# Optimization experiments

Measured on AMD Instinct MI355X. Metric: run time of the kernel, lower is better.

## Reference

```python
import jax, jax.numpy as jnp
import numpy as np

B, T, D_IN, D_OUT = 4, 2048, 1024, 1024


def setup_inputs() -> dict:
    key = jax.random.key(0)
    k0, k1, k2, k3 = jax.random.split(key, 4)
    token_embed = jax.random.normal(k0, (B, T, D_IN), dtype=jnp.float32)
    # torch Linear weight is [out, in]; store transposed [in, out] for x @ W
    Wq = jax.random.normal(k1, (D_IN, D_OUT), dtype=jnp.float32) * (1.0 / np.sqrt(D_IN))
    Wk = jax.random.normal(k2, (D_IN, D_OUT), dtype=jnp.float32) * (1.0 / np.sqrt(D_IN))
    Wv = jax.random.normal(k3, (D_IN, D_OUT), dtype=jnp.float32) * (1.0 / np.sqrt(D_IN))
    return {"token_embed": token_embed, "Wq": Wq, "Wk": Wk, "Wv": Wv}


def reference(token_embed, Wq, Wk, Wv):
    # token_embed: [B, T, d_in]
    num_token = token_embed.shape[1]
    q = jnp.einsum("btd,de->bte", token_embed, Wq)  # [B, T, d_out]
    k = jnp.einsum("btd,de->bte", token_embed, Wk)
    v = jnp.einsum("btd,de->bte", token_embed, Wv)
    scores = jnp.einsum("bqe,bke->bqk", q, k)  # [B, T, T]
    # causal mask: strictly-upper-triangular positions set to -inf
    causal = jnp.triu(jnp.ones((num_token, num_token), dtype=bool), k=1)
    scores = jnp.where(causal[None, :, :], -jnp.inf, scores)
    # NOTE: faithful to source bug: scale by sqrt(seq_len) (keys.shape[1]), not sqrt(d_out)
    scale = jnp.asarray(num_token, dtype=scores.dtype) ** 0.5
    attn = jax.nn.softmax(scores / scale, axis=-1)
    # dropout prob is 0 -> identity
    context = jnp.einsum("bqk,bke->bqe", attn, v)  # [B, T, d_out]
    return context
```

## Files before the change

kernel.cpp:

```cpp
#include <hip/hip_runtime.h>
#include <cstdint>
#include <cstddef>
#include <math.h>


typedef __attribute__((ext_vector_type(4))) float f32x4;
typedef __attribute__((ext_vector_type(8))) short s16x8;

#define AS1(p) ((const __attribute__((address_space(1))) void*)(p))
#define AS3(p) ((__attribute__((address_space(3))) void*)(p))
#define BARRIER() asm volatile("s_barrier" ::: "memory")
#define W8 asm volatile("s_waitcnt vmcnt(8)" ::: "memory")
#define W4 asm volatile("s_waitcnt vmcnt(4)" ::: "memory")
#define W0 asm volatile("s_waitcnt vmcnt(0)" ::: "memory")
#define LGKM0 do { asm volatile("s_waitcnt lgkmcnt(0)" ::: "memory"); \
                   __builtin_amdgcn_sched_barrier(0); } while (0)
#define WNONE ((void)0)
#define NOISSUE ((void)0)

static __device__ __forceinline__ unsigned short f2bf(float x) {
  unsigned int u = __float_as_uint(x);
  unsigned int r = u + 0x7FFFu + ((u >> 16) & 1u);
  return (unsigned short)(r >> 16);
}
static __device__ __forceinline__ float bf2f(unsigned short h) {
  return __uint_as_float(((unsigned int)h) << 16);
}

__global__ __launch_bounds__(256) void k_cvt(const float* __restrict__ X,
                                             const float* __restrict__ W0p,
                                             const float* __restrict__ W1p,
                                             const float* __restrict__ W2p,
                                             unsigned short* __restrict__ Xb,
                                             unsigned short* __restrict__ Wt) {
  __shared__ float tile[64][65];
  const int bx = blockIdx.x;
  if (bx < 4096) {
    size_t i = ((size_t)bx * 256 + threadIdx.x) * 8;
    float4 a = *(const float4*)(X + i);
    float4 b = *(const float4*)(X + i + 4);
    union { unsigned short us[8]; uint4 v; } o;
    o.us[0] = f2bf(a.x); o.us[1] = f2bf(a.y); o.us[2] = f2bf(a.z); o.us[3] = f2bf(a.w);
    o.us[4] = f2bf(b.x); o.us[5] = f2bf(b.y); o.us[6] = f2bf(b.z); o.us[7] = f2bf(b.w);
    *(uint4*)(Xb + i) = o.v;
    return;
  }
  const int bx2 = bx - 4096;
  const int z = bx2 >> 8, t = bx2 & 255;
  const float* W = z == 0 ? W0p : (z == 1 ? W1p : W2p);
  unsigned short* dst = Wt + (size_t)z * 1048576;
  const int k0 = (t >> 4) * 64, n0 = (t & 15) * 64;
  const int tr = threadIdx.x >> 4, tc = (threadIdx.x & 15) * 4;
  for (int i = 0; i < 4; ++i) {
    int r = tr + i * 16;
    float4 v = *(const float4*)(W + (size_t)(k0 + r) * 1024 + n0 + tc);
    tile[r][tc + 0] = v.x; tile[r][tc + 1] = v.y;
    tile[r][tc + 2] = v.z; tile[r][tc + 3] = v.w;
  }
  __syncthreads();
  for (int i = 0; i < 4; ++i) {
    int r = tr + i * 16;
    ushort4 o;
    o.x = f2bf(tile[tc + 0][r]); o.y = f2bf(tile[tc + 1][r]);
    o.z = f2bf(tile[tc + 2][r]); o.w = f2bf(tile[tc + 3][r]);
    *(ushort4*)(dst + (size_t)(n0 + r) * 1024 + k0 + tc) = o;
  }
}

static __device__ __forceinline__ void stage2(const char* src, size_t ld128, char* dst) {
  __builtin_amdgcn_global_load_lds(AS1(src), AS3(dst), 16, 0, 0);
  __builtin_amdgcn_global_load_lds(AS1(src + ld128), AS3(dst + 8192), 16, 0, 0);
}

template <class FA, class FB>
static __device__ __forceinline__ void core256(const char* __restrict__ As,
                                               const char* __restrict__ Bs,
                                               size_t ldA128, size_t ldB128,
                                               FA offA, FB offB,
                                               int nkt, char* smem, f32x4 (&acc)[8][4]) {
  const int tid = threadIdx.x, w = tid >> 6, lane = tid & 63;
  const int lr = lane & 15, lq = lane >> 4;
  const int wm = (w >> 2) * 128, wn = (w & 3) * 64;
  char* ldsA = smem + w * 1024;
  char* ldsB = smem + 65536 + w * 1024;
  s16x8 afA[4], afB[4], bfA[4], bfB[4];

#define STG_A(t, h) stage2(As + offA((t), (h)), ldA128, ldsA + (((t) & 1) * 2 + (h)) * 16384)
#define STG_B(t, h) stage2(Bs + offB((t), (h)), ldB128, ldsB + (((t) & 1) * 2 + (h)) * 16384)
#define RD_A(buf, h, r) (*(const s16x8*)(smem + ((buf) * 2 + (h)) * 16384 + (r) * 64 + ((lq ^ (((r) >> 1) & 3)) << 4)))
#define RD_B(buf, h, r) (*(const s16x8*)(smem + 65536 + ((buf) * 2 + (h)) * 16384 + (r) * 64 + ((lq ^ (((r) >> 1) & 3)) << 4)))
#define MMQ(AF, BF, base) \
  _Pragma("unroll") for (int i = 0; i < 4; ++i) \
  _Pragma("unroll") for (int c = 0; c < 4; ++c) \
    acc[(base) + i][c] = __builtin_amdgcn_mfma_f32_16x16x32_bf16(AF[i], BF[c], acc[(base) + i][c], 0, 0, 0)
#define PH_E(tt, hh, AFD, BFD, STG, WAIT) \
  _Pragma("unroll") for (int i = 0; i < 4; ++i) AFD[i] = RD_A((tt) & 1, hh, wm + i * 16 + lr); \
  _Pragma("unroll") for (int c = 0; c < 4; ++c) BFD[c] = RD_B((tt) & 1, hh, wn + c * 16 + lr); \
  STG; WAIT; BARRIER(); LGKM0; \
  __builtin_amdgcn_s_setprio(1); MMQ(AFD, BFD, 0); __builtin_amdgcn_s_setprio(0); \
  BARRIER();
#define PH_O(tt, hh, AFD, BFU, STG, WAIT) \
  _Pragma("unroll") for (int i = 0; i < 4; ++i) AFD[i] = RD_A((tt) & 1, hh, wm + 64 + i * 16 + lr); \
  STG; WAIT; BARRIER(); LGKM0; \
  __builtin_amdgcn_s_setprio(1); MMQ(AFD, BFU, 4); __builtin_amdgcn_s_setprio(0); \
  BARRIER();

  STG_A(0, 0); STG_B(0, 0);
  STG_A(0, 1); STG_B(0, 1);
  STG_A(1, 0); STG_B(1, 0);
  W8; BARRIER();

  const int niter = nkt >> 1;
  for (int I = 0; I < niter - 1; ++I) {
    const int t0 = 2 * I, t1 = 2 * I + 1;
    PH_E(t0, 0, afA, bfA, STG_A(t1, 1),     WNONE)
    PH_O(t0, 0, afB, bfA, STG_B(t1, 1),     W8)
    PH_E(t0, 1, afA, bfB, STG_A(t0 + 2, 0), WNONE)
    PH_O(t0, 1, afB, bfB, STG_B(t0 + 2, 0), W8)
    PH_E(t1, 0, afA, bfA, STG_A(t0 + 2, 1), WNONE)
    PH_O(t1, 0, afB, bfA, STG_B(t0 + 2, 1), W8)
    PH_E(t1, 1, afA, bfB, STG_A(t1 + 2, 0), WNONE)
    PH_O(t1, 1, afB, bfB, STG_B(t1 + 2, 0), W8)
  }
  {
    const int t0 = nkt - 2, t1 = nkt - 1;
    PH_E(t0, 0, afA, bfA, STG_A(t1, 1), WNONE)
    PH_O(t0, 0, afB, bfA, STG_B(t1, 1), W8)
    PH_E(t0, 1, afA, bfB, NOISSUE,      WNONE)
    PH_O(t0, 1, afB, bfB, NOISSUE,      W4)
    PH_E(t1, 0, afA, bfA, NOISSUE,      WNONE)
    PH_O(t1, 0, afB, bfA, NOISSUE,      W0)
    PH_E(t1, 1, afA, bfB, NOISSUE,      WNONE)
    PH_O(t1, 1, afB, bfB, NOISSUE,      WNONE)
  }

#undef STG_A
#undef STG_B
#undef RD_A
#undef RD_B
#undef MMQ
#undef PH_E
#undef PH_O
}

struct OffLinear {
  __device__ __forceinline__ size_t operator()(int t, int h) const {
    return (size_t)t * 128 + (size_t)h * 64;
  }
};
struct OffTriK {
  int k0;
  __device__ __forceinline__ size_t operator()(int t, int h) const {
    int g = k0 + t;
    return (size_t)(g >> 2) * 131072 + (size_t)(g & 3) * 128 + (size_t)h * 64;
  }
};
struct OffLinK {
  int k0;
  __device__ __forceinline__ size_t operator()(int t, int h) const {
    return (size_t)(k0 + t) * 128 + (size_t)h * 64;
  }
};

static __device__ __forceinline__ void lane_src(int& rowl, int& slot) {
  const int tid = threadIdx.x, w = tid >> 6, lane = tid & 63;
  rowl = w * 16 + (lane >> 2);
  slot = (lane & 3) ^ ((rowl >> 1) & 3);
}

__global__ __launch_bounds__(512, 2) void k_qk(const unsigned short* __restrict__ Xb,
                                               const unsigned short* __restrict__ Wt,
                                               unsigned short* __restrict__ Qm,
                                               unsigned short* __restrict__ Km) {
  __shared__ char smem[131072];
  const int by = blockIdx.y, z = by >> 2, q = by & 3, bx = blockIdx.x;
  const int m0 = bx * 256, n0 = q * 256;
  const char* A = (const char*)(Xb + (size_t)m0 * 1024);
  const char* B = (const char*)(Wt + (size_t)z * 1048576 + (size_t)n0 * 1024);
  int rowl, slot; lane_src(rowl, slot);
  const size_t lo = (size_t)rowl * 2048 + slot * 16;
  f32x4 acc[8][4];
#pragma unroll
  for (int i = 0; i < 8; ++i)
#pragma unroll
    for (int c = 0; c < 4; ++c) acc[i][c] = (f32x4){0.f, 0.f, 0.f, 0.f};
  core256(A + lo, B + lo, (size_t)128 * 2048, (size_t)128 * 2048,
          OffLinear{}, OffLinear{}, 16, smem, acc);
  unsigned short* C = z == 0 ? Qm : Km;
  const int tid = threadIdx.x, w = tid >> 6, lane = tid & 63;
  const int lr = lane & 15, lq = lane >> 4;
  const int wm = (w >> 2) * 128, wn = (w & 3) * 64;
#pragma unroll
  for (int fr = 0; fr < 8; ++fr)
#pragma unroll
    for (int fc = 0; fc < 4; ++fc)
#pragma unroll
      for (int i = 0; i < 4; ++i) {
        int row = m0 + wm + fr * 16 + lq * 4 + i;
        int col = n0 + wn + fc * 16 + lr;
        C[(size_t)row * 1024 + col] = f2bf(acc[fr][fc][i]);
      }
}

__global__ __launch_bounds__(512, 2) void k_v(const unsigned short* __restrict__ Xb,
                                              const unsigned short* __restrict__ Wt,
                                              unsigned short* __restrict__ Vt) {
  __shared__ char smem[131072];
  const int x = blockIdx.x;
  const int m0 = (x & 3) * 256, n0 = (x >> 2) * 256;
  const char* A = (const char*)(Wt + (size_t)2 * 1048576 + (size_t)m0 * 1024);
  const char* B = (const char*)(Xb + (size_t)n0 * 1024);
  int rowl, slot; lane_src(rowl, slot);
  const size_t lo = (size_t)rowl * 2048 + slot * 16;
  f32x4 acc[8][4];
#pragma unroll
  for (int a = 0; a < 8; ++a)
#pragma unroll
    for (int c = 0; c < 4; ++c) acc[a][c] = (f32x4){0.f, 0.f, 0.f, 0.f};
  core256(A + lo, B + lo, (size_t)128 * 2048, (size_t)128 * 2048,
          OffLinear{}, OffLinear{}, 16, smem, acc);
  const int tid = threadIdx.x, w = tid >> 6, lane = tid & 63;
  const int lr = lane & 15, lq = lane >> 4;
  const int wm = (w >> 2) * 128, wn = (w & 3) * 64;
#pragma unroll
  for (int fr = 0; fr < 8; ++fr)
#pragma unroll
    for (int fc = 0; fc < 4; ++fc)
#pragma unroll
      for (int i = 0; i < 4; ++i) {
        int row = m0 + wm + fr * 16 + lq * 4 + i;
        int col = n0 + wn + fc * 16 + lr;
        Vt[((size_t)(col >> 11) * 1024 + row) * 2048 + (col & 2047)] = f2bf(acc[fr][fc][i]);
      }
}

__global__ __launch_bounds__(512, 2) void k_sg(const unsigned short* __restrict__ Qm,
                                               const unsigned short* __restrict__ Km,
                                               unsigned short* __restrict__ S) {
  __shared__ char smem[131072];
  const int id = blockIdx.x;
  int i = 0;
  while ((i + 1) * (i + 2) / 2 <= id) ++i;
  const int j = id - i * (i + 1) / 2;
  const int b = blockIdx.y;
  const int m0 = i * 256, n0 = j * 256;
  int rowl, slot; lane_src(rowl, slot);
  const size_t lo = (size_t)rowl * 2048 + slot * 16;
  f32x4 acc[8][4];
#pragma unroll
  for (int a = 0; a < 8; ++a)
#pragma unroll
    for (int c = 0; c < 4; ++c) acc[a][c] = (f32x4){0.f, 0.f, 0.f, 0.f};
  core256((const char*)(Qm + ((size_t)b * 2048 + m0) * 1024) + lo,
          (const char*)(Km + ((size_t)b * 2048 + n0) * 1024) + lo,
          (size_t)128 * 2048, (size_t)128 * 2048, OffLinear{}, OffLinear{}, 16, smem, acc);
  const float SCALE = 0.022097086912079608f;
  const int tid = threadIdx.x, w = tid >> 6, lane = tid & 63;
  const int lr = lane & 15, lq = lane >> 4;
  const int wm = (w >> 2) * 128, wn = (w & 3) * 64;
  unsigned short* tb = S + (((size_t)(b * 36 + id)) << 16);
#pragma unroll
  for (int fr = 0; fr < 8; ++fr)
#pragma unroll
    for (int fc = 0; fc < 4; ++fc)
#pragma unroll
      for (int i2 = 0; i2 < 4; ++i2) {
        int rl = wm + fr * 16 + lq * 4 + i2;
        int cl = wn + fc * 16 + lr;
        tb[(size_t)rl * 256 + cl] = f2bf(acc[fr][fc][i2] * SCALE);
      }
}

__global__ __launch_bounds__(256) void k_softmax(unsigned short* __restrict__ S) {
  const int tid = threadIdx.x, w = tid >> 6, lane = tid & 63;
  const int row = blockIdx.x * 4 + w;
  const int b = row >> 11, q = row & 2047;
  const int i = q >> 8, ntl = i + 1, rowL = q & 255;
  unsigned short* base = S + (((size_t)(b * 36 + (i * (i + 1)) / 2)) << 16)
                           + (size_t)rowL * 256 + lane * 4;
  float v[8][4];
#pragma unroll
  for (int t = 0; t < 8; ++t) {
    if (t < ntl) {
      ushort4 x = *(const ushort4*)(base + (size_t)t * 65536);
      int c0 = t * 256 + lane * 4;
      v[t][0] = (c0 + 0 <= q) ? bf2f(x.x) : -INFINITY;
      v[t][1] = (c0 + 1 <= q) ? bf2f(x.y) : -INFINITY;
      v[t][2] = (c0 + 2 <= q) ? bf2f(x.z) : -INFINITY;
      v[t][3] = (c0 + 3 <= q) ? bf2f(x.w) : -INFINITY;
    } else {
      v[t][0] = v[t][1] = v[t][2] = v[t][3] = -INFINITY;
    }
  }
  float m = -INFINITY;
#pragma unroll
  for (int t = 0; t < 8; ++t)
#pragma unroll
    for (int jj = 0; jj < 4; ++jj) m = fmaxf(m, v[t][jj]);
  for (int off = 32; off; off >>= 1) m = fmaxf(m, __shfl_xor(m, off));
  float s = 0.f;
#pragma unroll
  for (int t = 0; t < 8; ++t)
#pragma unroll
    for (int jj = 0; jj < 4; ++jj) { v[t][jj] = __expf(v[t][jj] - m); s += v[t][jj]; }
  for (int off = 32; off; off >>= 1) s += __shfl_xor(s, off);
  const float inv = 1.f / s;
#pragma unroll
  for (int t = 0; t < 8; ++t)
    if (t < ntl) {
      ushort4 o;
      o.x = f2bf(v[t][0] * inv); o.y = f2bf(v[t][1] * inv);
      o.z = f2bf(v[t][2] * inv); o.w = f2bf(v[t][3] * inv);
      *(ushort4*)(base + (size_t)t * 65536) = o;
    }
}

__device__ const int pvi[15] = {2, 5, 5, 7, 7, 4, 4, 6, 6, 1, 3, 3, 6, 7, 0};
__device__ const int pvk[15] = {0, 0, 12, 0, 12, 0, 10, 0, 10, 0, 0, 8, 20, 24, 0};
__device__ const int pvn[15] = {12, 12, 12, 12, 12, 10, 10, 10, 10, 8, 8, 8, 8, 8, 4};
__device__ const int pvp[15] = {-1, -1, 2, -1, 5, -1, 1, -1, 3, -1, -1, 0, 4, 6, -1};

__global__ __launch_bounds__(512, 2) void k_pv(const unsigned short* __restrict__ P,
                                               const unsigned short* __restrict__ Vt,
                                               float* __restrict__ out,
                                               float* __restrict__ part) {
  __shared__ char smem[131072];
  const int cx = blockIdx.x % 15;
  const int panel = blockIdx.x / 15;
  const int nt = panel & 3, b = panel >> 2;
  const int i = pvi[cx], k0 = pvk[cx], nkt = pvn[cx], psl = pvp[cx];
  const char* Pb = (const char*)P + (((size_t)(b * 36 + (i * (i + 1)) / 2)) << 17);
  int rowl, slot; lane_src(rowl, slot);
  const char* Asrc = Pb + (size_t)rowl * 512 + slot * 16;
  const char* Bsrc = (const char*)Vt + ((size_t)(b * 1024 + nt * 256 + rowl)) * 4096 + slot * 16;
  f32x4 acc[8][4];
#pragma unroll
  for (int a = 0; a < 8; ++a)
#pragma unroll
    for (int c = 0; c < 4; ++c) acc[a][c] = (f32x4){0.f, 0.f, 0.f, 0.f};
  core256(Asrc, Bsrc, (size_t)128 * 512, (size_t)128 * 4096,
          OffTriK{k0}, OffLinK{k0}, nkt, smem, acc);
  const int tid = threadIdx.x, w = tid >> 6, lane = tid & 63;
  const int lr = lane & 15, lq = lane >> 4;
  const int wm = (w >> 2) * 128, wn = (w & 3) * 64;
  if (psl < 0) {
#pragma unroll
    for (int fr = 0; fr < 8; ++fr)
#pragma unroll
      for (int fc = 0; fc < 4; ++fc)
#pragma unroll
        for (int i2 = 0; i2 < 4; ++i2) {
          int orow = i * 256 + wm + fr * 16 + lq * 4 + i2;
          int col = nt * 256 + wn + fc * 16 + lr;
          out[((size_t)b * 2048 + orow) * 1024 + col] = acc[fr][fc][i2];
        }
  } else {
    float* pt = part + ((size_t)(panel * 7 + psl)) * 65536;
#pragma unroll
    for (int fr = 0; fr < 8; ++fr)
#pragma unroll
      for (int fc = 0; fc < 4; ++fc)
#pragma unroll
        for (int i2 = 0; i2 < 4; ++i2) {
          int rl = wm + fr * 16 + lq * 4 + i2;
          int cl = wn + fc * 16 + lr;
          pt[(size_t)rl * 256 + cl] = acc[fr][fc][i2];
        }
  }
}

__global__ __launch_bounds__(256) void k_fix(float* __restrict__ out,
                                             const float* __restrict__ part) {
  const size_t e = ((size_t)blockIdx.x * 256 + threadIdx.x) * 4;
  const int b = (int)(e / 1310720);
  const int rem = (int)(e % 1310720);
  const int row = 768 + (rem >> 10);
  const int col = rem & 1023;
  const int i = row >> 8;
  const int nt = col >> 8;
  const int base4[5] = {0, 1, 2, 3, 5};
  const int cnt4[5] = {1, 1, 1, 2, 2};
  const int sb = base4[i - 3], cnt = cnt4[i - 3];
  const float* pt = part + ((size_t)((b * 4 + nt) * 7 + sb)) * 65536
                         + (size_t)(row & 255) * 256 + (col & 255);
  float* op = out + ((size_t)b * 2048 + row) * 1024 + col;
  float4 o = *(const float4*)op;
  float4 p0 = *(const float4*)pt;
  o.x += p0.x; o.y += p0.y; o.z += p0.z; o.w += p0.w;
  if (cnt == 2) {
    float4 p1 = *(const float4*)(pt + 65536);
    o.x += p1.x; o.y += p1.y; o.z += p1.z; o.w += p1.w;
  }
  *(float4*)op = o;
}

extern "C" void kernel_launch(void* const* d_in, const int* in_sizes, int n_in,
                              void* d_out, int out_size, void* d_ws, size_t ws_size,
                              hipStream_t stream) {
  const float* X  = (const float*)d_in[0];
  const float* W0p = (const float*)d_in[1];
  const float* W1p = (const float*)d_in[2];
  const float* W2p = (const float*)d_in[3];
  float* out = (float*)d_out;
  char* ws = (char*)d_ws;
  unsigned short* Xb = (unsigned short*)ws;
  unsigned short* Wt = (unsigned short*)(ws + (size_t)16777216);
  unsigned short* Qm = (unsigned short*)(ws + (size_t)23068672);
  unsigned short* Km = (unsigned short*)(ws + (size_t)39845888);
  unsigned short* Vt = (unsigned short*)(ws + (size_t)56623104);
  unsigned short* Sb = (unsigned short*)ws;
  float* Pp = (float*)(ws + (size_t)23068672);
  (void)in_sizes; (void)n_in; (void)out_size; (void)ws_size;

  hipLaunchKernelGGL(k_cvt, dim3(4864), dim3(256), 0, stream, X, W0p, W1p, W2p, Xb, Wt);
  hipLaunchKernelGGL(k_qk, dim3(32, 8), dim3(512), 0, stream, Xb, Wt, Qm, Km);
  hipLaunchKernelGGL(k_v, dim3(128), dim3(512), 0, stream, Xb, Wt, Vt);
  hipLaunchKernelGGL(k_sg, dim3(36, 4), dim3(512), 0, stream, Qm, Km, Sb);
  hipLaunchKernelGGL(k_softmax, dim3(2048), dim3(256), 0, stream, Sb);
  hipLaunchKernelGGL(k_pv, dim3(240), dim3(512), 0, stream, Sb, Vt, out, Pp);
  hipLaunchKernelGGL(k_fix, dim3(5120), dim3(256), 0, stream, out, Pp);
}
```

Measured before the change: 164.5 us.

## Restructure GEMM core to simple double-buffered 64-wide k-tiles with 128B-row swizzle

Replaces the half-tile (32-wide) staged pipeline, which kept three half-stages in flight with fine-grained vmcnt waits, with a plain double buffer of full 64-wide k-tiles. Each k-step issues four global-to-LDS loads per operand for the next tile, then fully drains (vmcnt 0) at the end of the step. The LDS layout moves to 128-byte rows with an 8-way XOR swizzle, and lane-to-address mapping changes to match. This simplifies the schedule and may change bank-conflict behaviour. The cost is shallower prefetch, since each iteration waits for all outstanding loads, so less latency can be hidden.

```diff
diff --git a/kernel.cpp b/kernel.cpp
--- a/kernel.cpp
+++ b/kernel.cpp
@@ -10,13 +10,9 @@
 #define AS1(p) ((const __attribute__((address_space(1))) void*)(p))
 #define AS3(p) ((__attribute__((address_space(3))) void*)(p))
 #define BARRIER() asm volatile("s_barrier" ::: "memory")
-#define W8 asm volatile("s_waitcnt vmcnt(8)" ::: "memory")
-#define W4 asm volatile("s_waitcnt vmcnt(4)" ::: "memory")
 #define W0 asm volatile("s_waitcnt vmcnt(0)" ::: "memory")
 #define LGKM0 do { asm volatile("s_waitcnt lgkmcnt(0)" ::: "memory"); \
                    __builtin_amdgcn_sched_barrier(0); } while (0)
-#define WNONE ((void)0)
-#define NOISSUE ((void)0)
 
 static __device__ __forceinline__ unsigned short f2bf(float x) {
   unsigned int u = __float_as_uint(x);
@@ -67,71 +63,69 @@
   }
 }
 
-static __device__ __forceinline__ void stage2(const char* src, size_t ld128, char* dst) {
-  __builtin_amdgcn_global_load_lds(AS1(src), AS3(dst), 16, 0, 0);
-  __builtin_amdgcn_global_load_lds(AS1(src + ld128), AS3(dst + 8192), 16, 0, 0);
-}
-
 template <class FA, class FB>
 static __device__ __forceinline__ void core256(const char* __restrict__ As,
                                                const char* __restrict__ Bs,
-                                               size_t ldA128, size_t ldB128,
+                                               size_t ldA, size_t ldB,
                                                FA offA, FB offB,
                                                int nkt, char* smem, f32x4 (&acc)[8][4]) {
   const int tid = threadIdx.x, w = tid >> 6, lane = tid & 63;
   const int lr = lane & 15, lq = lane >> 4;
   const int wm = (w >> 2) * 128, wn = (w & 3) * 64;
-  char* ldsA = smem + w * 1024;
-  char* ldsB = smem + 65536 + w * 1024;
+  char* ldsA = smem + w * 4096;
+  char* ldsB = smem + 65536 + w * 4096;
   s16x8 afA[4], afB[4], bfA[4], bfB[4];
 
-#define STG_A(t, h) stage2(As + offA((t), (h)), ldA128, ldsA + (((t) & 1) * 2 + (h)) * 16384)
-#define STG_B(t, h) stage2(Bs + offB((t), (h)), ldB128, ldsB + (((t) & 1) * 2 + (h)) * 16384)
-#define RD_A(buf, h, r) (*(const s16x8*)(smem + ((buf) * 2 + (h)) * 16384 + (r) * 64 + ((lq ^ (((r) >> 1) & 3)) << 4)))
-#define RD_B(buf, h, r) (*(const s16x8*)(smem + 65536 + ((buf) * 2 + (h)) * 16384 + (r) * 64 + ((lq ^ (((r) >> 1) & 3)) << 4)))
+#define STG_A(t) do { char* _d = ldsA + ((t) & 1) * 32768; const char* _s = As + offA(t); \
+    __builtin_amdgcn_global_load_lds(AS1(_s), AS3(_d), 16, 0, 0); \
+    __builtin_amdgcn_global_load_lds(AS1(_s + 8 * ldA), AS3(_d + 1024), 16, 0, 0); \
+    __builtin_amdgcn_global_load_lds(AS1(_s + 16 * ldA), AS3(_d + 2048), 16, 0, 0); \
+    __builtin_amdgcn_global_load_lds(AS1(_s + 24 * ldA), AS3(_d + 3072), 16, 0, 0); } while (0)
+#define STG_B(t) do { char* _d = ldsB + ((t) & 1) * 32768; const char* _s = Bs + offB(t); \
+    __builtin_amdgcn_global_load_lds(AS1(_s), AS3(_d), 16, 0, 0); \
+    __builtin_amdgcn_global_load_lds(AS1(_s + 8 * ldB), AS3(_d + 1024), 16, 0, 0); \
+    __builtin_amdgcn_global_load_lds(AS1(_s + 16 * ldB), AS3(_d + 2048), 16, 0, 0); \
+    __builtin_amdgcn_global_load_lds(AS1(_s + 24 * ldB), AS3(_d + 3072), 16, 0, 0); } while (0)
+#define RD_A(buf, h, r) (*(const s16x8*)(smem + (buf) * 32768 + (size_t)(r) * 128 + ((((((h) << 2) | lq)) ^ ((r) & 7)) << 4)))
+#define RD_B(buf, h, r) (*(const s16x8*)(smem + 65536 + (buf) * 32768 + (size_t)(r) * 128 + ((((((h) << 2) | lq)) ^ ((r) & 7)) << 4)))
 #define MMQ(AF, BF, base) \
   _Pragma("unroll") for (int i = 0; i < 4; ++i) \
   _Pragma("unroll") for (int c = 0; c < 4; ++c) \
     acc[(base) + i][c] = __builtin_amdgcn_mfma_f32_16x16x32_bf16(AF[i], BF[c], acc[(base) + i][c], 0, 0, 0)
-#define PH_E(tt, hh, AFD, BFD, STG, WAIT) \
-  _Pragma("unroll") for (int i = 0; i < 4; ++i) AFD[i] = RD_A((tt) & 1, hh, wm + i * 16 + lr); \
-  _Pragma("unroll") for (int c = 0; c < 4; ++c) BFD[c] = RD_B((tt) & 1, hh, wn + c * 16 + lr); \
-  STG; WAIT; BARRIER(); LGKM0; \
-  __builtin_amdgcn_s_setprio(1); MMQ(AFD, BFD, 0); __builtin_amdgcn_s_setprio(0); \
-  BARRIER();
-#define PH_O(tt, hh, AFD, BFU, STG, WAIT) \
-  _Pragma("unroll") for (int i = 0; i < 4; ++i) AFD[i] = RD_A((tt) & 1, hh, wm + 64 + i * 16 + lr); \
-  STG; WAIT; BARRIER(); LGKM0; \
-  __builtin_amdgcn_s_setprio(1); MMQ(AFD, BFU, 4); __builtin_amdgcn_s_setprio(0); \
-  BARRIER();
-
-  STG_A(0, 0); STG_B(0, 0);
-  STG_A(0, 1); STG_B(0, 1);
-  STG_A(1, 0); STG_B(1, 0);
-  W8; BARRIER();
-
-  const int niter = nkt >> 1;
-  for (int I = 0; I < niter - 1; ++I) {
-    const int t0 = 2 * I, t1 = 2 * I + 1;
-    PH_E(t0, 0, afA, bfA, STG_A(t1, 1),     WNONE)
-    PH_O(t0, 0, afB, bfA, STG_B(t1, 1),     W8)
-    PH_E(t0, 1, afA, bfB, STG_A(t0 + 2, 0), WNONE)
-    PH_O(t0, 1, afB, bfB, STG_B(t0 + 2, 0), W8)
-    PH_E(t1, 0, afA, bfA, STG_A(t0 + 2, 1), WNONE)
-    PH_O(t1, 0, afB, bfA, STG_B(t0 + 2, 1), W8)
-    PH_E(t1, 1, afA, bfB, STG_A(t1 + 2, 0), WNONE)
-    PH_O(t1, 1, afB, bfB, STG_B(t1 + 2, 0), W8)
-  }
-  {
-    const int t0 = nkt - 2, t1 = nkt - 1;
-    PH_E(t0, 0, afA, bfA, STG_A(t1, 1), WNONE)
-    PH_O(t0, 0, afB, bfA, STG_B(t1, 1), W8)
-    PH_E(t0, 1, afA, bfB, NOISSUE,      WNONE)
-    PH_O(t0, 1, afB, bfB, NOISSUE,      W4)
-    PH_E(t1, 0, afA, bfA, NOISSUE,      WNONE)
-    PH_O(t1, 0, afB, bfA, NOISSUE,      W0)
-    PH_E(t1, 1, afA, bfB, NOISSUE,      WNONE)
-    PH_O(t1, 1, afB, bfB, NOISSUE,      WNONE)
+
+  STG_A(0); STG_B(0);
+  W0; BARRIER();
+
+  for (int t = 0; t < nkt; ++t) {
+    const int buf = t & 1;
+    const bool more = (t + 1) < nkt;
+#pragma unroll
+    for (int i = 0; i < 4; ++i) afA[i] = RD_A(buf, 0, wm + i * 16 + lr);
+#pragma unroll
+    for (int c = 0; c < 4; ++c) bfA[c] = RD_B(buf, 0, wn + c * 16 + lr);
+    if (more) STG_A(t + 1);
+    BARRIER(); LGKM0;
+    __builtin_amdgcn_s_setprio(1); MMQ(afA, bfA, 0); __builtin_amdgcn_s_setprio(0);
+    BARRIER();
+#pragma unroll
+    for (int i = 0; i < 4; ++i) afB[i] = RD_A(buf, 0, wm + 64 + i * 16 + lr);
+    if (more) STG_B(t + 1);
+    BARRIER(); LGKM0;
+    __builtin_amdgcn_s_setprio(1); MMQ(afB, bfA, 4); __builtin_amdgcn_s_setprio(0);
+    BARRIER();
+#pragma unroll
+    for (int i = 0; i < 4; ++i) afA[i] = RD_A(buf, 1, wm + i * 16 + lr);
+#pragma unroll
+    for (int c = 0; c < 4; ++c) bfB[c] = RD_B(buf, 1, wn + c * 16 + lr);
+    BARRIER(); LGKM0;
+    __builtin_amdgcn_s_setprio(1); MMQ(afA, bfB, 0); __builtin_amdgcn_s_setprio(0);
+    BARRIER();
+#pragma unroll
+    for (int i = 0; i < 4; ++i) afB[i] = RD_A(buf, 1, wm + 64 + i * 16 + lr);
+    BARRIER(); LGKM0;
+    __builtin_amdgcn_s_setprio(1); MMQ(afB, bfB, 4); __builtin_amdgcn_s_setprio(0);
+    if (more) { W0; }
+    BARRIER();
   }
 
 #undef STG_A
@@ -139,33 +133,31 @@
 #undef RD_A
 #undef RD_B
 #undef MMQ
-#undef PH_E
-#undef PH_O
 }
 
 struct OffLinear {
-  __device__ __forceinline__ size_t operator()(int t, int h) const {
-    return (size_t)t * 128 + (size_t)h * 64;
+  __device__ __forceinline__ size_t operator()(int t) const {
+    return (size_t)t * 128;
   }
 };
 struct OffTriK {
   int k0;
-  __device__ __forceinline__ size_t operator()(int t, int h) const {
+  __device__ __forceinline__ size_t operator()(int t) const {
     int g = k0 + t;
-    return (size_t)(g >> 2) * 131072 + (size_t)(g & 3) * 128 + (size_t)h * 64;
+    return (size_t)(g >> 2) * 131072 + (size_t)(g & 3) * 128;
   }
 };
 struct OffLinK {
   int k0;
-  __device__ __forceinline__ size_t operator()(int t, int h) const {
-    return (size_t)(k0 + t) * 128 + (size_t)h * 64;
+  __device__ __forceinline__ size_t operator()(int t) const {
+    return (size_t)(k0 + t) * 128;
   }
 };
 
-static __device__ __forceinline__ void lane_src(int& rowl, int& slot) {
-  const int tid = threadIdx.x, w = tid >> 6, lane = tid & 63;
-  rowl = w * 16 + (lane >> 2);
-  slot = (lane & 3) ^ ((rowl >> 1) & 3);
+static __device__ __forceinline__ void lane_src(int& rowl, int& chunk) {
+  const int tid = threadIdx.x, w = tid >> 6, lane = tid & 63;
+  rowl = w * 32 + (lane >> 3);
+  chunk = (lane & 7) ^ (lane >> 3);
 }
 
 __global__ __launch_bounds__(512, 2) void k_qk(const unsigned short* __restrict__ Xb,
@@ -177,15 +169,14 @@
   const int m0 = bx * 256, n0 = q * 256;
   const char* A = (const char*)(Xb + (size_t)m0 * 1024);
   const char* B = (const char*)(Wt + (size_t)z * 1048576 + (size_t)n0 * 1024);
-  int rowl, slot; lane_src(rowl, slot);
-  const size_t lo = (size_t)rowl * 2048 + slot * 16;
+  int rowl, chunk; lane_src(rowl, chunk);
+  const size_t lo = (size_t)rowl * 2048 + chunk * 16;
   f32x4 acc[8][4];
 #pragma unroll
   for (int i = 0; i < 8; ++i)
 #pragma unroll
     for (int c = 0; c < 4; ++c) acc[i][c] = (f32x4){0.f, 0.f, 0.f, 0.f};
-  core256(A + lo, B + lo, (size_t)128 * 2048, (size_t)128 * 2048,
-          OffLinear{}, OffLinear{}, 16, smem, acc);
+  core256(A + lo, B + lo, 2048, 2048, OffLinear{}, OffLinear{}, 16, smem, acc);
   unsigned short* C = z == 0 ? Qm : Km;
   const int tid = threadIdx.x, w = tid >> 6, lane = tid & 63;
   const int lr = lane & 15, lq = lane >> 4;
@@ -210,15 +201,14 @@
   const int m0 = (x & 3) * 256, n0 = (x >> 2) * 256;
   const char* A = (const char*)(Wt + (size_t)2 * 1048576 + (size_t)m0 * 1024);
   const char* B = (const char*)(Xb + (size_t)n0 * 1024);
-  int rowl, slot; lane_src(rowl, slot);
-  const size_t lo = (size_t)rowl * 2048 + slot * 16;
+  int rowl, chunk; lane_src(rowl, chunk);
+  const size_t lo = (size_t)rowl * 2048 + chunk * 16;
   f32x4 acc[8][4];
 #pragma unroll
   for (int a = 0; a < 8; ++a)
 #pragma unroll
     for (int c = 0; c < 4; ++c) acc[a][c] = (f32x4){0.f, 0.f, 0.f, 0.f};
-  core256(A + lo, B + lo, (size_t)128 * 2048, (size_t)128 * 2048,
-          OffLinear{}, OffLinear{}, 16, smem, acc);
+  core256(A + lo, B + lo, 2048, 2048, OffLinear{}, OffLinear{}, 16, smem, acc);
   const int tid = threadIdx.x, w = tid >> 6, lane = tid & 63;
   const int lr = lane & 15, lq = lane >> 4;
   const int wm = (w >> 2) * 128, wn = (w & 3) * 64;
@@ -244,8 +234,8 @@
   const int j = id - i * (i + 1) / 2;
   const int b = blockIdx.y;
   const int m0 = i * 256, n0 = j * 256;
-  int rowl, slot; lane_src(rowl, slot);
-  const size_t lo = (size_t)rowl * 2048 + slot * 16;
+  int rowl, chunk; lane_src(rowl, chunk);
+  const size_t lo = (size_t)rowl * 2048 + chunk * 16;
   f32x4 acc[8][4];
 #pragma unroll
   for (int a = 0; a < 8; ++a)
@@ -253,7 +243,7 @@
     for (int c = 0; c < 4; ++c) acc[a][c] = (f32x4){0.f, 0.f, 0.f, 0.f};
   core256((const char*)(Qm + ((size_t)b * 2048 + m0) * 1024) + lo,
           (const char*)(Km + ((size_t)b * 2048 + n0) * 1024) + lo,
-          (size_t)128 * 2048, (size_t)128 * 2048, OffLinear{}, OffLinear{}, 16, smem, acc);
+          2048, 2048, OffLinear{}, OffLinear{}, 16, smem, acc);
   const float SCALE = 0.022097086912079608f;
   const int tid = threadIdx.x, w = tid >> 6, lane = tid & 63;
   const int lr = lane & 15, lq = lane >> 4;
@@ -330,16 +320,15 @@
   const int nt = panel & 3, b = panel >> 2;
   const int i = pvi[cx], k0 = pvk[cx], nkt = pvn[cx], psl = pvp[cx];
   const char* Pb = (const char*)P + (((size_t)(b * 36 + (i * (i + 1)) / 2)) << 17);
-  int rowl, slot; lane_src(rowl, slot);
-  const char* Asrc = Pb + (size_t)rowl * 512 + slot * 16;
-  const char* Bsrc = (const char*)Vt + ((size_t)(b * 1024 + nt * 256 + rowl)) * 4096 + slot * 16;
+  int rowl, chunk; lane_src(rowl, chunk);
+  const char* Asrc = Pb + (size_t)rowl * 512 + chunk * 16;
+  const char* Bsrc = (const char*)Vt + ((size_t)(b * 1024 + nt * 256 + rowl)) * 4096 + chunk * 16;
   f32x4 acc[8][4];
 #pragma unroll
   for (int a = 0; a < 8; ++a)
 #pragma unroll
     for (int c = 0; c < 4; ++c) acc[a][c] = (f32x4){0.f, 0.f, 0.f, 0.f};
-  core256(Asrc, Bsrc, (size_t)128 * 512, (size_t)128 * 4096,
-          OffTriK{k0}, OffLinK{k0}, nkt, smem, acc);
+  core256(Asrc, Bsrc, 512, 4096, OffTriK{k0}, OffLinK{k0}, nkt, smem, acc);
   const int tid = threadIdx.x, w = tid >> 6, lane = tid & 63;
   const int lr = lane & 15, lq = lane >> 4;
   const int wm = (w >> 2) * 128, wn = (w & 3) * 64;
```

Measured after the change: 168.9 us. 2.7% more time.

## Restructure GEMM core pipeline into single-barrier half-tile phases with split LDS waits

Applied to the files above, without the earlier changes.

Replaces the even/odd sub-phase schedule (two barriers per sub-phase, A and B staged separately) with one phase per half-tile. Each phase loads all A and B fragments, issues the next half-tile's A and B staging together, and uses a single barrier. A partial lgkmcnt wait lets the first MFMA block start while the second half of the A fragments is still arriving. This cuts barrier count and keeps fewer fragment registers live. In exchange, global-to-LDS prefetch distance drops from several half-tiles ahead to one, so load latency may be less hidden.

```diff
diff --git a/kernel.cpp b/kernel.cpp
--- a/kernel.cpp
+++ b/kernel.cpp
@@ -10,11 +10,10 @@
 #define AS1(p) ((const __attribute__((address_space(1))) void*)(p))
 #define AS3(p) ((__attribute__((address_space(3))) void*)(p))
 #define BARRIER() asm volatile("s_barrier" ::: "memory")
-#define W8 asm volatile("s_waitcnt vmcnt(8)" ::: "memory")
 #define W4 asm volatile("s_waitcnt vmcnt(4)" ::: "memory")
-#define W0 asm volatile("s_waitcnt vmcnt(0)" ::: "memory")
-#define LGKM0 do { asm volatile("s_waitcnt lgkmcnt(0)" ::: "memory"); \
-                   __builtin_amdgcn_sched_barrier(0); } while (0)
+#define W0c asm volatile("s_waitcnt vmcnt(0)" ::: "memory")
+#define LGKM(n) do { asm volatile("s_waitcnt lgkmcnt(" #n ")" ::: "memory"); \
+                     __builtin_amdgcn_sched_barrier(0); } while (0)
 #define WNONE ((void)0)
 #define NOISSUE ((void)0)
 
@@ -83,64 +82,49 @@
   const int wm = (w >> 2) * 128, wn = (w & 3) * 64;
   char* ldsA = smem + w * 1024;
   char* ldsB = smem + 65536 + w * 1024;
-  s16x8 afA[4], afB[4], bfA[4], bfB[4];
+  s16x8 afA[4], afB[4], bfr[4];
 
 #define STG_A(t, h) stage2(As + offA((t), (h)), ldA128, ldsA + (((t) & 1) * 2 + (h)) * 16384)
 #define STG_B(t, h) stage2(Bs + offB((t), (h)), ldB128, ldsB + (((t) & 1) * 2 + (h)) * 16384)
+#define STG(t, h) do { STG_A(t, h); STG_B(t, h); } while (0)
 #define RD_A(buf, h, r) (*(const s16x8*)(smem + ((buf) * 2 + (h)) * 16384 + (r) * 64 + ((lq ^ (((r) >> 1) & 3)) << 4)))
 #define RD_B(buf, h, r) (*(const s16x8*)(smem + 65536 + ((buf) * 2 + (h)) * 16384 + (r) * 64 + ((lq ^ (((r) >> 1) & 3)) << 4)))
 #define MMQ(AF, BF, base) \
   _Pragma("unroll") for (int i = 0; i < 4; ++i) \
   _Pragma("unroll") for (int c = 0; c < 4; ++c) \
     acc[(base) + i][c] = __builtin_amdgcn_mfma_f32_16x16x32_bf16(AF[i], BF[c], acc[(base) + i][c], 0, 0, 0)
-#define PH_E(tt, hh, AFD, BFD, STG, WAIT) \
-  _Pragma("unroll") for (int i = 0; i < 4; ++i) AFD[i] = RD_A((tt) & 1, hh, wm + i * 16 + lr); \
-  _Pragma("unroll") for (int c = 0; c < 4; ++c) BFD[c] = RD_B((tt) & 1, hh, wn + c * 16 + lr); \
-  STG; WAIT; BARRIER(); LGKM0; \
-  __builtin_amdgcn_s_setprio(1); MMQ(AFD, BFD, 0); __builtin_amdgcn_s_setprio(0); \
-  BARRIER();
-#define PH_O(tt, hh, AFD, BFU, STG, WAIT) \
-  _Pragma("unroll") for (int i = 0; i < 4; ++i) AFD[i] = RD_A((tt) & 1, hh, wm + 64 + i * 16 + lr); \
-  STG; WAIT; BARRIER(); LGKM0; \
-  __builtin_amdgcn_s_setprio(1); MMQ(AFD, BFU, 4); __builtin_amdgcn_s_setprio(0); \
-  BARRIER();
-
-  STG_A(0, 0); STG_B(0, 0);
-  STG_A(0, 1); STG_B(0, 1);
-  STG_A(1, 0); STG_B(1, 0);
-  W8; BARRIER();
-
-  const int niter = nkt >> 1;
-  for (int I = 0; I < niter - 1; ++I) {
-    const int t0 = 2 * I, t1 = 2 * I + 1;
-    PH_E(t0, 0, afA, bfA, STG_A(t1, 1),     WNONE)
-    PH_O(t0, 0, afB, bfA, STG_B(t1, 1),     W8)
-    PH_E(t0, 1, afA, bfB, STG_A(t0 + 2, 0), WNONE)
-    PH_O(t0, 1, afB, bfB, STG_B(t0 + 2, 0), W8)
-    PH_E(t1, 0, afA, bfA, STG_A(t0 + 2, 1), WNONE)
-    PH_O(t1, 0, afB, bfA, STG_B(t0 + 2, 1), W8)
-    PH_E(t1, 1, afA, bfB, STG_A(t1 + 2, 0), WNONE)
-    PH_O(t1, 1, afB, bfB, STG_B(t1 + 2, 0), W8)
-  }
-  {
-    const int t0 = nkt - 2, t1 = nkt - 1;
-    PH_E(t0, 0, afA, bfA, STG_A(t1, 1), WNONE)
-    PH_O(t0, 0, afB, bfA, STG_B(t1, 1), W8)
-    PH_E(t0, 1, afA, bfB, NOISSUE,      WNONE)
-    PH_O(t0, 1, afB, bfB, NOISSUE,      W4)
-    PH_E(t1, 0, afA, bfA, NOISSUE,      WNONE)
-    PH_O(t1, 0, afB, bfA, NOISSUE,      W0)
-    PH_E(t1, 1, afA, bfB, NOISSUE,      WNONE)
-    PH_O(t1, 1, afB, bfB, NOISSUE,      WNONE)
-  }
+#define PHASE(TT, HH, ISSUE, WVM) { \
+    const int _bf = (TT) & 1; \
+    _Pragma("unroll") for (int i = 0; i < 4; ++i) afA[i] = RD_A(_bf, HH, wm + i * 16 + lr); \
+    _Pragma("unroll") for (int c = 0; c < 4; ++c) bfr[c] = RD_B(_bf, HH, wn + c * 16 + lr); \
+    _Pragma("unroll") for (int i = 0; i < 4; ++i) afB[i] = RD_A(_bf, HH, wm + 64 + i * 16 + lr); \
+    ISSUE; WVM; BARRIER(); \
+    LGKM(4); \
+    __builtin_amdgcn_s_setprio(1); \
+    MMQ(afA, bfr, 0); \
+    LGKM(0); \
+    MMQ(afB, bfr, 4); \
+    __builtin_amdgcn_s_setprio(0); \
+  }
+
+  STG(0, 0); STG(0, 1);
+  W4; BARRIER();
+
+  int t = 0;
+  for (; t + 1 < nkt; ++t) {
+    PHASE(t, 0, STG(t + 1, 0), W4)
+    PHASE(t, 1, STG(t + 1, 1), W4)
+  }
+  PHASE(t, 0, NOISSUE, W0c)
+  PHASE(t, 1, NOISSUE, WNONE)
 
 #undef STG_A
 #undef STG_B
+#undef STG
 #undef RD_A
 #undef RD_B
 #undef MMQ
-#undef PH_E
-#undef PH_O
+#undef PHASE
 }
 
 struct OffLinear {
```

Measured after the change: 161.7 us. About the same (-1.7%).
